# Kernel tuning notes

Measured on AMD Instinct MI355X. Metric: run time of the kernel, lower is better.

The kernel has to match this reference:

```python
import jax, jax.numpy as jnp
import numpy as np
import math

LAMBDA_INIT = 0.8 - 0.6 * math.exp(-0.3 * 2)  # depth=2


def setup_inputs() -> dict:
    key = jax.random.key(0)
    ks = jax.random.split(key, 10)
    B, T, E, hd = 1, 2048, 1024, 32
    s = 0.02
    return {
        "x": jax.random.normal(ks[0], (B, T, E), jnp.float32),
        "Wq": jax.random.normal(ks[1], (E, E), jnp.float32) * s,
        "Wk": jax.random.normal(ks[2], (E, E), jnp.float32) * s,
        "Wv": jax.random.normal(ks[3], (E, E), jnp.float32) * s,
        "Wo": jax.random.normal(ks[4], (E, E), jnp.float32) * s,
        "lambda_q1": jax.random.normal(ks[5], (hd,), jnp.float32) * 0.1,
        "lambda_k1": jax.random.normal(ks[6], (hd,), jnp.float32) * 0.1,
        "lambda_q2": jax.random.normal(ks[7], (hd,), jnp.float32) * 0.1,
        "lambda_k2": jax.random.normal(ks[8], (hd,), jnp.float32) * 0.1,
        "gamma": jnp.ones((2 * hd,), jnp.float32),
    }


def reference(x, Wq, Wk, Wv, Wo, lambda_q1, lambda_k1, lambda_q2, lambda_k2, gamma):
    B, T, E = x.shape
    hd = gamma.shape[0] // 2          # head_dim
    H = E // (2 * hd)                 # num_heads
    scaling = hd ** -0.5

    # projections (torch Linear: y = x @ W.T)
    q = (x @ Wq.T).reshape(B, T, 2 * H, hd).transpose(0, 2, 1, 3)  # [B,2H,T,hd]
    k = (x @ Wk.T).reshape(B, T, 2 * H, hd).transpose(0, 2, 1, 3)  # [B,2H,T,hd]
    v = (x @ Wv.T).reshape(B, T, H, 2 * hd).transpose(0, 2, 1, 3)  # [B,H,T,2hd]

    # causal mask (offset = 0 since src_len == tgt_len)
    mask = jnp.triu(jnp.full((T, T), -jnp.inf, jnp.float32), k=1)

    attn_weights = jnp.einsum('bhtd,bhsd->bhts', q * scaling, k) + mask
    attn_weights = jax.nn.softmax(attn_weights.astype(jnp.float32), axis=-1).astype(x.dtype)

    lambda_1 = jnp.exp(jnp.sum(lambda_q1 * lambda_k1).astype(jnp.float32))
    lambda_2 = jnp.exp(jnp.sum(lambda_q2 * lambda_k2).astype(jnp.float32))
    lambda_full = (lambda_1 - lambda_2 + LAMBDA_INIT).astype(x.dtype)

    aw = attn_weights.reshape(B, H, 2, T, T)
    diff = aw[:, :, 0] - lambda_full * aw[:, :, 1]          # [B,H,T,T]

    attn = jnp.einsum('bhts,bhsd->bhtd', diff, v)            # [B,H,T,2hd]

    # RMSNorm over last dim (computed in fp32)
    a32 = attn.astype(jnp.float32)
    normed = a32 * jax.lax.rsqrt(jnp.mean(a32 * a32, axis=-1, keepdims=True) + 1e-5)
    attn = gamma * normed.astype(attn.dtype)
    attn = attn * (1 - LAMBDA_INIT)

    attn = attn.transpose(0, 2, 1, 3).reshape(B, T, E)
    return attn @ Wo.T
```

## Files before the change

### kernel.cpp

```cpp
#include <hip/hip_runtime.h>
#include <math.h>

typedef float f32x4 __attribute__((ext_vector_type(4)));
typedef __bf16 bf16x8 __attribute__((ext_vector_type(8)));

#define MFMA16(a, b, c) __builtin_amdgcn_mfma_f32_16x16x32_bf16((a), (b), (c), 0, 0, 0)

__device__ __forceinline__ unsigned short f2bf(float f) {
    union { float f; unsigned u; } v; v.f = f;
    return (unsigned short)((v.u + 0x7fffu + ((v.u >> 16) & 1u)) >> 16);
}
__device__ __forceinline__ unsigned pack2(float a, float b) {
    return (unsigned)f2bf(a) | ((unsigned)f2bf(b) << 16);
}

__global__ __launch_bounds__(256)
void convert_bf16(const float* __restrict__ x,  const float* __restrict__ wq,
                  const float* __restrict__ wk, const float* __restrict__ wv,
                  const float* __restrict__ wo,
                  unsigned short* __restrict__ xb,  unsigned short* __restrict__ wqb,
                  unsigned short* __restrict__ wkb, unsigned short* __restrict__ wvb,
                  unsigned short* __restrict__ wob)
{
    int i = blockIdx.x * 256 + threadIdx.x;
    const float* s; unsigned short* d; int o;
    if (i < 524288)       { s = x;  d = xb;  o = i; }
    else if (i < 786432)  { s = wq; d = wqb; o = i - 524288; }
    else if (i < 1048576) { s = wk; d = wkb; o = i - 786432; }
    else if (i < 1310720) { s = wv; d = wvb; o = i - 1048576; }
    else                  { s = wo; d = wob; o = i - 1310720; }
    float4 v = *reinterpret_cast<const float4*>(s + (size_t)o * 4);
    ushort4 r;
    r.x = f2bf(v.x); r.y = f2bf(v.y); r.z = f2bf(v.z); r.w = f2bf(v.w);
    *reinterpret_cast<ushort4*>(d + (size_t)o * 4) = r;
}

__device__ __forceinline__ void gemm_bf16_body(const unsigned short* __restrict__ A,
                                               const unsigned short* __restrict__ W,
                                               void* __restrict__ Cp, int mode)
{
    __shared__ char Al[128 * 128];
    __shared__ char Bl[64 * 128];

    const int tid = threadIdx.x;
    const int lane = tid & 63, w = tid >> 6;
    const int g = lane >> 4, r15 = lane & 15;
    const int wm = (w >> 1) * 64, wn = (w & 1) * 32;
    const int m0 = blockIdx.y * 128, n0 = blockIdx.x * 64;

    f32x4 acc[4][2] = {};

    for (int k0 = 0; k0 < 1024; k0 += 64) {
        __syncthreads();
#pragma unroll
        for (int p = 0; p < 4; p++) {
            int idx = p * 256 + tid;
            int row = idx >> 3, c8 = idx & 7;
            bf16x8 v = *reinterpret_cast<const bf16x8*>(A + (size_t)(m0 + row) * 1024 + k0 + c8 * 8);
            int byte = (row * 128 + c8 * 16) ^ ((row & 7) << 4);
            *reinterpret_cast<bf16x8*>(Al + byte) = v;
        }
#pragma unroll
        for (int p = 0; p < 2; p++) {
            int idx = p * 256 + tid;
            int row = idx >> 3, c8 = idx & 7;
            bf16x8 v = *reinterpret_cast<const bf16x8*>(W + (size_t)(n0 + row) * 1024 + k0 + c8 * 8);
            int byte = (row * 128 + c8 * 16) ^ ((row & 7) << 4);
            *reinterpret_cast<bf16x8*>(Bl + byte) = v;
        }
        __syncthreads();
#pragma unroll
        for (int c = 0; c < 2; c++) {
            bf16x8 af[4], bfr[2];
#pragma unroll
            for (int m = 0; m < 4; m++) {
                int row = wm + m * 16 + r15;
                int byte = (row * 128 + g * 16 + c * 64) ^ ((row & 7) << 4);
                af[m] = *reinterpret_cast<const bf16x8*>(Al + byte);
            }
#pragma unroll
            for (int n = 0; n < 2; n++) {
                int row = wn + n * 16 + r15;
                int byte = (row * 128 + g * 16 + c * 64) ^ ((row & 7) << 4);
                bfr[n] = *reinterpret_cast<const bf16x8*>(Bl + byte);
            }
#pragma unroll
            for (int m = 0; m < 4; m++)
#pragma unroll
                for (int n = 0; n < 2; n++)
                    acc[m][n] = MFMA16(af[m], bfr[n], acc[m][n]);
        }
    }

    if (mode == 0) {
        unsigned short* C = (unsigned short*)Cp;
#pragma unroll
        for (int m = 0; m < 4; m++)
#pragma unroll
            for (int n = 0; n < 2; n++)
#pragma unroll
                for (int i = 0; i < 4; i++)
                    C[(size_t)(m0 + wm + m * 16 + g * 4 + i) * 1024 + n0 + wn + n * 16 + r15] =
                        f2bf(acc[m][n][i]);
    } else if (mode == 1) {
        unsigned short* C = (unsigned short*)Cp;
#pragma unroll
        for (int m = 0; m < 4; m++)
#pragma unroll
            for (int n = 0; n < 2; n++) {
                unsigned long long v = (unsigned long long)pack2(acc[m][n][0], acc[m][n][1])
                                     | ((unsigned long long)pack2(acc[m][n][2], acc[m][n][3]) << 32);
                *reinterpret_cast<unsigned long long*>(
                    C + (size_t)(n0 + wn + n * 16 + r15) * 2048 + m0 + wm + m * 16 + g * 4) = v;
            }
    } else {
        float* C = (float*)Cp;
#pragma unroll
        for (int m = 0; m < 4; m++)
#pragma unroll
            for (int n = 0; n < 2; n++)
#pragma unroll
                for (int i = 0; i < 4; i++)
                    C[(size_t)(m0 + wm + m * 16 + g * 4 + i) * 1024 + n0 + wn + n * 16 + r15] =
                        acc[m][n][i];
    }
}

__global__ __launch_bounds__(256)
void gemm_qkv_bf16(const unsigned short* __restrict__ xb, const unsigned short* __restrict__ wqb,
                   const unsigned short* __restrict__ wkb, const unsigned short* __restrict__ wvb,
                   unsigned short* __restrict__ Qb, unsigned short* __restrict__ Kb,
                   unsigned short* __restrict__ Vtb)
{
    int z = blockIdx.z;
    const unsigned short* W = (z == 0) ? wqb : (z == 1) ? wkb : wvb;
    void* C = (z == 0) ? (void*)Qb : (z == 1) ? (void*)Kb : (void*)Vtb;
    gemm_bf16_body(xb, W, C, (z == 2) ? 1 : 0);
}

__global__ __launch_bounds__(256)
void gemm_out_bf16(const unsigned short* __restrict__ Nb, const unsigned short* __restrict__ wob,
                   float* __restrict__ out)
{
    gemm_bf16_body(Nb, wob, out, 2);
}

__global__ __launch_bounds__(256)
void attn_mfma(const unsigned short* __restrict__ Qb, const unsigned short* __restrict__ Kb,
               const unsigned short* __restrict__ Vtb, unsigned short* __restrict__ Nb,
               const float* __restrict__ lq1, const float* __restrict__ lk1,
               const float* __restrict__ lq2, const float* __restrict__ lk2,
               const float* __restrict__ gamma)
{
    __shared__ char Kl[64 * 128];
    __shared__ char Vl[64 * 128];
    __shared__ char Pl[2][64 * 128];

    const int tid = threadIdx.x, lane = tid & 63, w = tid >> 6;
    const int g = lane >> 4, r15 = lane & 15;
    const int u = blockIdx.x >> 4, h = blockIdx.x & 15;
    const int qb = (u < 16) ? u : 47 - u;
    const int q0 = qb * 64;
    const int row_g = q0 + w * 16 + r15;

    float s1 = 0.f, s2 = 0.f;
#pragma unroll
    for (int i = 0; i < 32; i++) { s1 += lq1[i] * lk1[i]; s2 += lq2[i] * lk2[i]; }
    const float LI = 0.4707130183435841f;
    const float lam = expf(s1) - expf(s2) + LI;
    const float scale = 0.17677669529663687f;

    bf16x8 qf0 = *reinterpret_cast<const bf16x8*>(Qb + (size_t)row_g * 1024 + h * 64 + g * 8);
    bf16x8 qf1 = *reinterpret_cast<const bf16x8*>(Qb + (size_t)row_g * 1024 + h * 64 + 32 + g * 8);

    f32x4 oacc[2][4] = {};
    float m_r[2] = {-INFINITY, -INFINITY};
    float l_r[2] = {0.f, 0.f};

    for (int kb = 0; kb <= qb; kb++) {
        const int j0 = kb * 64;
        __syncthreads();
#pragma unroll
        for (int p = 0; p < 2; p++) {
            int idx = p * 256 + tid;
            int row = idx >> 3, c8 = idx & 7;
            bf16x8 v = *reinterpret_cast<const bf16x8*>(Kb + (size_t)(j0 + row) * 1024 + h * 64 + c8 * 8);
            int byte = (row * 128 + c8 * 16) ^ ((row & 7) << 4);
            *reinterpret_cast<bf16x8*>(Kl + byte) = v;
        }
#pragma unroll
        for (int p = 0; p < 2; p++) {
            int idx = p * 256 + tid;
            int row = idx >> 3, c8 = idx & 7;
            bf16x8 v = *reinterpret_cast<const bf16x8*>(Vtb + (size_t)(h * 64 + row) * 2048 + j0 + c8 * 8);
            int byte = (row * 128 + c8 * 16) ^ ((row & 7) << 4);
            *reinterpret_cast<bf16x8*>(Vl + byte) = v;
        }
        __syncthreads();

        f32x4 sc0[4] = {}, sc1[4] = {};
#pragma unroll
        for (int m = 0; m < 4; m++) {
            int row = m * 16 + r15;
            int b0 = (row * 128 + g * 16) ^ ((row & 7) << 4);
            int b1 = (row * 128 + g * 16 + 64) ^ ((row & 7) << 4);
            bf16x8 a0 = *reinterpret_cast<const bf16x8*>(Kl + b0);
            bf16x8 a1 = *reinterpret_cast<const bf16x8*>(Kl + b1);
            sc0[m] = MFMA16(a0, qf0, sc0[m]);
            sc1[m] = MFMA16(a1, qf1, sc1[m]);
        }

        const bool diag = (kb == qb);
        float corr[2];
#pragma unroll
        for (int s = 0; s < 2; s++) {
            f32x4* sc = s ? sc1 : sc0;
            float sv[4][4];
            float mx = -INFINITY;
#pragma unroll
            for (int m = 0; m < 4; m++)
#pragma unroll
                for (int i = 0; i < 4; i++) {
                    float xv = sc[m][i] * scale;
                    if (diag && (j0 + m * 16 + g * 4 + i) > row_g) xv = -INFINITY;
                    sv[m][i] = xv;
                    mx = fmaxf(mx, xv);
                }
            mx = fmaxf(mx, __shfl_xor(mx, 16));
            mx = fmaxf(mx, __shfl_xor(mx, 32));
            const float mn = fmaxf(m_r[s], mx);
            corr[s] = __expf(m_r[s] - mn);
            m_r[s] = mn;
            float sum = 0.f;
            const int prow = w * 16 + r15;
#pragma unroll
            for (int m = 0; m < 4; m++) {
                float p0 = __expf(sv[m][0] - mn);
                float p1 = __expf(sv[m][1] - mn);
                float p2 = __expf(sv[m][2] - mn);
                float p3 = __expf(sv[m][3] - mn);
                sum += (p0 + p1) + (p2 + p3);
                unsigned long long pv = (unsigned long long)pack2(p0, p1)
                                      | ((unsigned long long)pack2(p2, p3) << 32);
                int byte = (prow * 128 + m * 32 + g * 8) ^ ((prow & 7) << 4);
                *reinterpret_cast<unsigned long long*>(Pl[s] + byte) = pv;
            }
            sum += __shfl_xor(sum, 16);
            sum += __shfl_xor(sum, 32);
            l_r[s] = l_r[s] * corr[s] + sum;
        }

        float c0[4], c1v[4];
#pragma unroll
        for (int i = 0; i < 4; i++) {
            c0[i]  = __shfl(corr[0], g * 4 + i);
            c1v[i] = __shfl(corr[1], g * 4 + i);
        }
#pragma unroll
        for (int n = 0; n < 4; n++)
#pragma unroll
            for (int i = 0; i < 4; i++) {
                oacc[0][n][i] *= c0[i];
                oacc[1][n][i] *= c1v[i];
            }

#pragma unroll
        for (int c = 0; c < 2; c++) {
            const int prow = w * 16 + r15;
            int pb = (prow * 128 + g * 16 + c * 64) ^ ((prow & 7) << 4);
            bf16x8 p0 = *reinterpret_cast<const bf16x8*>(Pl[0] + pb);
            bf16x8 p1 = *reinterpret_cast<const bf16x8*>(Pl[1] + pb);
#pragma unroll
            for (int n = 0; n < 4; n++) {
                int vrow = n * 16 + r15;
                int vb = (vrow * 128 + g * 16 + c * 64) ^ ((vrow & 7) << 4);
                bf16x8 vf = *reinterpret_cast<const bf16x8*>(Vl + vb);
                oacc[0][n] = MFMA16(p0, vf, oacc[0][n]);
                oacc[1][n] = MFMA16(p1, vf, oacc[1][n]);
            }
        }
    }

    float i1[4], i2[4];
    {
        float r1 = 1.f / l_r[0];
        float r2 = lam / l_r[1];
#pragma unroll
        for (int i = 0; i < 4; i++) {
            i1[i] = __shfl(r1, g * 4 + i);
            i2[i] = __shfl(r2, g * 4 + i);
        }
    }
    float o[4][4], ss[4] = {0.f, 0.f, 0.f, 0.f};
#pragma unroll
    for (int n = 0; n < 4; n++)
#pragma unroll
        for (int i = 0; i < 4; i++) {
            float v = oacc[0][n][i] * i1[i] - oacc[1][n][i] * i2[i];
            o[n][i] = v;
            ss[i] = fmaf(v, v, ss[i]);
        }
#pragma unroll
    for (int i = 0; i < 4; i++) {
        ss[i] += __shfl_xor(ss[i], 1);
        ss[i] += __shfl_xor(ss[i], 2);
        ss[i] += __shfl_xor(ss[i], 4);
        ss[i] += __shfl_xor(ss[i], 8);
    }
    const float post = 1.f - LI;
    float gm4[4];
#pragma unroll
    for (int n = 0; n < 4; n++) gm4[n] = gamma[n * 16 + r15];
#pragma unroll
    for (int i = 0; i < 4; i++) {
        const float rs = rsqrtf(ss[i] * 0.015625f + 1e-5f);
#pragma unroll
        for (int n = 0; n < 4; n++) {
            Nb[(size_t)(q0 + w * 16 + g * 4 + i) * 1024 + h * 64 + n * 16 + r15] =
                f2bf(o[n][i] * rs * gm4[n] * post);
        }
    }
}

extern "C" void kernel_launch(void* const* d_in, const int* in_sizes, int n_in,
                              void* d_out, int out_size, void* d_ws, size_t ws_size,
                              hipStream_t stream)
{
    const float* x   = (const float*)d_in[0];
    const float* Wq  = (const float*)d_in[1];
    const float* Wk  = (const float*)d_in[2];
    const float* Wv  = (const float*)d_in[3];
    const float* Wo  = (const float*)d_in[4];
    const float* lq1 = (const float*)d_in[5];
    const float* lk1 = (const float*)d_in[6];
    const float* lq2 = (const float*)d_in[7];
    const float* lk2 = (const float*)d_in[8];
    const float* gm  = (const float*)d_in[9];
    float* out = (float*)d_out;

    unsigned short* ws  = (unsigned short*)d_ws;
    unsigned short* xb  = ws;
    unsigned short* wqb = xb  + 2097152;
    unsigned short* wkb = wqb + 1048576;
    unsigned short* wvb = wkb + 1048576;
    unsigned short* wob = wvb + 1048576;
    unsigned short* Qb  = wob + 1048576;
    unsigned short* Kb  = Qb  + 2097152;
    unsigned short* Vtb = Kb  + 2097152;
    unsigned short* Nb  = Vtb + 2097152;

    convert_bf16<<<6144, 256, 0, stream>>>(x, Wq, Wk, Wv, Wo, xb, wqb, wkb, wvb, wob);
    gemm_qkv_bf16<<<dim3(16, 16, 3), 256, 0, stream>>>(xb, wqb, wkb, wvb, Qb, Kb, Vtb);
    attn_mfma<<<512, 256, 0, stream>>>(Qb, Kb, Vtb, Nb, lq1, lk1, lq2, lk2, gm);
    gemm_out_bf16<<<dim3(16, 16), 256, 0, stream>>>(Nb, wob, out);
}
```

Before: 195.5 us.

## Fold softmax scale into Q, use lazy exp2 rescaling, halve attention query tile

Q is pre-scaled by scale*log2(e) in the QKV GEMM epilogue, so the attention kernel can use exp2 with no per-element scale multiply. Online softmax now rescales only when a wave's row max grows by more than 8 (in log2 units), and row sums are reduced only once at the end. The attention grid uses 32-row query tiles with 128 threads and 1024 blocks to improve load balance and occupancy, at the cost of loading each K/V tile twice as often.

```diff
diff --git a/kernel.cpp b/kernel.cpp
--- a/kernel.cpp
+++ b/kernel.cpp
@@ -92,7 +92,8 @@
         }
     }
 
-    if (mode == 0) {
+    if (mode == 0 || mode == 3) {
+        const float cs = (mode == 3) ? 0.25504190132624806f : 1.0f;
         unsigned short* C = (unsigned short*)Cp;
 #pragma unroll
         for (int m = 0; m < 4; m++)
@@ -101,7 +102,7 @@
 #pragma unroll
                 for (int i = 0; i < 4; i++)
                     C[(size_t)(m0 + wm + m * 16 + g * 4 + i) * 1024 + n0 + wn + n * 16 + r15] =
-                        f2bf(acc[m][n][i]);
+                        f2bf(acc[m][n][i] * cs);
     } else if (mode == 1) {
         unsigned short* C = (unsigned short*)Cp;
 #pragma unroll
@@ -135,7 +136,7 @@
     int z = blockIdx.z;
     const unsigned short* W = (z == 0) ? wqb : (z == 1) ? wkb : wvb;
     void* C = (z == 0) ? (void*)Qb : (z == 1) ? (void*)Kb : (void*)Vtb;
-    gemm_bf16_body(xb, W, C, (z == 2) ? 1 : 0);
+    gemm_bf16_body(xb, W, C, (z == 2) ? 1 : (z == 0 ? 3 : 0));
 }
 
 __global__ __launch_bounds__(256)
@@ -145,52 +146,53 @@
     gemm_bf16_body(Nb, wob, out, 2);
 }
 
-__global__ __launch_bounds__(256)
-void attn_mfma(const unsigned short* __restrict__ Qb, const unsigned short* __restrict__ Kb,
-               const unsigned short* __restrict__ Vtb, unsigned short* __restrict__ Nb,
-               const float* __restrict__ lq1, const float* __restrict__ lk1,
-               const float* __restrict__ lq2, const float* __restrict__ lk2,
-               const float* __restrict__ gamma)
+__global__ __launch_bounds__(128)
+void attn_mfma2(const unsigned short* __restrict__ Qb, const unsigned short* __restrict__ Kb,
+                const unsigned short* __restrict__ Vtb, unsigned short* __restrict__ Nb,
+                const float* __restrict__ lq1, const float* __restrict__ lk1,
+                const float* __restrict__ lq2, const float* __restrict__ lk2,
+                const float* __restrict__ gamma)
 {
     __shared__ char Kl[64 * 128];
     __shared__ char Vl[64 * 128];
-    __shared__ char Pl[2][64 * 128];
+    __shared__ char Pl[2][32 * 128];
 
     const int tid = threadIdx.x, lane = tid & 63, w = tid >> 6;
     const int g = lane >> 4, r15 = lane & 15;
     const int u = blockIdx.x >> 4, h = blockIdx.x & 15;
-    const int qb = (u < 16) ? u : 47 - u;
-    const int q0 = qb * 64;
+    const int qb = (u < 32) ? u : 95 - u;
+    const int q0 = qb * 32;
     const int row_g = q0 + w * 16 + r15;
+    const int prow  = w * 16 + r15;
 
     float s1 = 0.f, s2 = 0.f;
 #pragma unroll
     for (int i = 0; i < 32; i++) { s1 += lq1[i] * lk1[i]; s2 += lq2[i] * lk2[i]; }
     const float LI = 0.4707130183435841f;
     const float lam = expf(s1) - expf(s2) + LI;
-    const float scale = 0.17677669529663687f;
 
     bf16x8 qf0 = *reinterpret_cast<const bf16x8*>(Qb + (size_t)row_g * 1024 + h * 64 + g * 8);
     bf16x8 qf1 = *reinterpret_cast<const bf16x8*>(Qb + (size_t)row_g * 1024 + h * 64 + 32 + g * 8);
 
     f32x4 oacc[2][4] = {};
-    float m_r[2] = {-INFINITY, -INFINITY};
-    float l_r[2] = {0.f, 0.f};
-
-    for (int kb = 0; kb <= qb; kb++) {
+    float m_u[2] = {-INFINITY, -INFINITY};
+    float l_l[2] = {0.f, 0.f};
+
+    const int nkb = (qb + 2) >> 1;
+    for (int kb = 0; kb < nkb; kb++) {
         const int j0 = kb * 64;
         __syncthreads();
 #pragma unroll
-        for (int p = 0; p < 2; p++) {
-            int idx = p * 256 + tid;
+        for (int p = 0; p < 4; p++) {
+            int idx = p * 128 + tid;
             int row = idx >> 3, c8 = idx & 7;
             bf16x8 v = *reinterpret_cast<const bf16x8*>(Kb + (size_t)(j0 + row) * 1024 + h * 64 + c8 * 8);
             int byte = (row * 128 + c8 * 16) ^ ((row & 7) << 4);
             *reinterpret_cast<bf16x8*>(Kl + byte) = v;
         }
 #pragma unroll
-        for (int p = 0; p < 2; p++) {
-            int idx = p * 256 + tid;
+        for (int p = 0; p < 4; p++) {
+            int idx = p * 128 + tid;
             int row = idx >> 3, c8 = idx & 7;
             bf16x8 v = *reinterpret_cast<const bf16x8*>(Vtb + (size_t)(h * 64 + row) * 2048 + j0 + c8 * 8);
             int byte = (row * 128 + c8 * 16) ^ ((row & 7) << 4);
@@ -210,63 +212,64 @@
             sc1[m] = MFMA16(a1, qf1, sc1[m]);
         }
 
-        const bool diag = (kb == qb);
-        float corr[2];
+        const bool diag = (kb == nkb - 1);
 #pragma unroll
         for (int s = 0; s < 2; s++) {
             f32x4* sc = s ? sc1 : sc0;
             float sv[4][4];
-            float mx = -INFINITY;
-#pragma unroll
-            for (int m = 0; m < 4; m++)
-#pragma unroll
-                for (int i = 0; i < 4; i++) {
-                    float xv = sc[m][i] * scale;
-                    if (diag && (j0 + m * 16 + g * 4 + i) > row_g) xv = -INFINITY;
-                    sv[m][i] = xv;
-                    mx = fmaxf(mx, xv);
-                }
-            mx = fmaxf(mx, __shfl_xor(mx, 16));
-            mx = fmaxf(mx, __shfl_xor(mx, 32));
-            const float mn = fmaxf(m_r[s], mx);
-            corr[s] = __expf(m_r[s] - mn);
-            m_r[s] = mn;
+            float mxl = -INFINITY;
+            if (diag) {
+#pragma unroll
+                for (int m = 0; m < 4; m++)
+#pragma unroll
+                    for (int i = 0; i < 4; i++) {
+                        float xv = ((j0 + m * 16 + g * 4 + i) <= row_g) ? sc[m][i] : -INFINITY;
+                        sv[m][i] = xv;
+                        mxl = fmaxf(mxl, xv);
+                    }
+            } else {
+#pragma unroll
+                for (int m = 0; m < 4; m++)
+#pragma unroll
+                    for (int i = 0; i < 4; i++) {
+                        sv[m][i] = sc[m][i];
+                        mxl = fmaxf(mxl, sc[m][i]);
+                    }
+            }
+            if (__any(mxl > m_u[s] + 8.0f)) {
+                float wm = mxl;
+                wm = fmaxf(wm, __shfl_xor(wm, 1));
+                wm = fmaxf(wm, __shfl_xor(wm, 2));
+                wm = fmaxf(wm, __shfl_xor(wm, 4));
+                wm = fmaxf(wm, __shfl_xor(wm, 8));
+                wm = fmaxf(wm, __shfl_xor(wm, 16));
+                wm = fmaxf(wm, __shfl_xor(wm, 32));
+                const float corr = exp2f(m_u[s] - wm);
+                m_u[s] = wm;
+                l_l[s] *= corr;
+#pragma unroll
+                for (int n = 0; n < 4; n++)
+#pragma unroll
+                    for (int i = 0; i < 4; i++) oacc[s][n][i] *= corr;
+            }
             float sum = 0.f;
-            const int prow = w * 16 + r15;
 #pragma unroll
             for (int m = 0; m < 4; m++) {
-                float p0 = __expf(sv[m][0] - mn);
-                float p1 = __expf(sv[m][1] - mn);
-                float p2 = __expf(sv[m][2] - mn);
-                float p3 = __expf(sv[m][3] - mn);
+                float p0 = exp2f(sv[m][0] - m_u[s]);
+                float p1 = exp2f(sv[m][1] - m_u[s]);
+                float p2 = exp2f(sv[m][2] - m_u[s]);
+                float p3 = exp2f(sv[m][3] - m_u[s]);
                 sum += (p0 + p1) + (p2 + p3);
                 unsigned long long pv = (unsigned long long)pack2(p0, p1)
                                       | ((unsigned long long)pack2(p2, p3) << 32);
                 int byte = (prow * 128 + m * 32 + g * 8) ^ ((prow & 7) << 4);
                 *reinterpret_cast<unsigned long long*>(Pl[s] + byte) = pv;
             }
-            sum += __shfl_xor(sum, 16);
-            sum += __shfl_xor(sum, 32);
-            l_r[s] = l_r[s] * corr[s] + sum;
-        }
-
-        float c0[4], c1v[4];
-#pragma unroll
-        for (int i = 0; i < 4; i++) {
-            c0[i]  = __shfl(corr[0], g * 4 + i);
-            c1v[i] = __shfl(corr[1], g * 4 + i);
-        }
-#pragma unroll
-        for (int n = 0; n < 4; n++)
-#pragma unroll
-            for (int i = 0; i < 4; i++) {
-                oacc[0][n][i] *= c0[i];
-                oacc[1][n][i] *= c1v[i];
-            }
+            l_l[s] += sum;
+        }
 
 #pragma unroll
         for (int c = 0; c < 2; c++) {
-            const int prow = w * 16 + r15;
             int pb = (prow * 128 + g * 16 + c * 64) ^ ((prow & 7) << 4);
             bf16x8 p0 = *reinterpret_cast<const bf16x8*>(Pl[0] + pb);
             bf16x8 p1 = *reinterpret_cast<const bf16x8*>(Pl[1] + pb);
@@ -281,15 +284,17 @@
         }
     }
 
+    float l0 = l_l[0];
+    l0 += __shfl_xor(l0, 16); l0 += __shfl_xor(l0, 32);
+    float l1 = l_l[1];
+    l1 += __shfl_xor(l1, 16); l1 += __shfl_xor(l1, 32);
+    const float r1 = 1.f / l0;
+    const float r2 = lam / l1;
     float i1[4], i2[4];
-    {
-        float r1 = 1.f / l_r[0];
-        float r2 = lam / l_r[1];
-#pragma unroll
-        for (int i = 0; i < 4; i++) {
-            i1[i] = __shfl(r1, g * 4 + i);
-            i2[i] = __shfl(r2, g * 4 + i);
-        }
+#pragma unroll
+    for (int i = 0; i < 4; i++) {
+        i1[i] = __shfl(r1, g * 4 + i);
+        i2[i] = __shfl(r2, g * 4 + i);
     }
     float o[4][4], ss[4] = {0.f, 0.f, 0.f, 0.f};
 #pragma unroll
@@ -351,6 +356,6 @@
 
     convert_bf16<<<6144, 256, 0, stream>>>(x, Wq, Wk, Wv, Wo, xb, wqb, wkb, wvb, wob);
     gemm_qkv_bf16<<<dim3(16, 16, 3), 256, 0, stream>>>(xb, wqb, wkb, wvb, Qb, Kb, Vtb);
-    attn_mfma<<<512, 256, 0, stream>>>(Qb, Kb, Vtb, Nb, lq1, lk1, lq2, lk2, gm);
+    attn_mfma2<<<1024, 128, 0, stream>>>(Qb, Kb, Vtb, Nb, lq1, lk1, lq2, lk2, gm);
     gemm_out_bf16<<<dim3(16, 16), 256, 0, stream>>>(Nb, wob, out);
 }
```

After: 192.0 us. Within noise of the previous version (-1.8%).
